# Kernel optimization log

Hardware: AMD Instinct MI355X
Metric: run time of the kernel (lower is better)

## Reference

```python
import jax, jax.numpy as jnp
import numpy as np

N_NODES = 131072
N_EDGES = 4194304
NUM_GRAPHS = 128


def setup_inputs() -> dict:
    key = jax.random.key(0)
    ks = jax.random.split(key, 12)
    x = jax.random.normal(ks[0], (N_NODES, 3), dtype=jnp.float32)
    edge_index = jax.random.randint(ks[1], (2, N_EDGES), 0, N_NODES, dtype=jnp.int32)
    batch = jnp.sort(jax.random.randint(ks[2], (N_NODES,), 0, NUM_GRAPHS, dtype=jnp.int32))
    W1 = jax.random.normal(ks[3], (3, 16), dtype=jnp.float32) * 0.5
    b1 = jax.random.normal(ks[4], (16,), dtype=jnp.float32) * 0.1
    W2 = jax.random.normal(ks[5], (16, 64), dtype=jnp.float32) * 0.25
    b2 = jax.random.normal(ks[6], (64,), dtype=jnp.float32) * 0.1
    fcw1 = jax.random.normal(ks[7], (64, 32), dtype=jnp.float32) * 0.125
    fcb1 = jax.random.normal(ks[8], (32,), dtype=jnp.float32) * 0.1
    fcw2 = jax.random.normal(ks[9], (32, 2), dtype=jnp.float32) * 0.2
    fcb2 = jax.random.normal(ks[10], (2,), dtype=jnp.float32) * 0.1
    return dict(x=x, edge_index=edge_index, batch=batch, W1=W1, b1=b1,
                W2=W2, b2=b2, fcw1=fcw1, fcb1=fcb1, fcw2=fcw2, fcb2=fcb2)


def _gcn_conv(x, W, b, src, dst, n_nodes):
    # PyG GCNConv: add self-loops, symmetric D^-1/2 A_hat D^-1/2, then scatter-add at dst.
    h = x @ W  # [N, out]
    deg = jax.ops.segment_sum(jnp.ones_like(dst, dtype=h.dtype), dst, num_segments=n_nodes)
    dinv = jnp.where(deg > 0, jax.lax.rsqrt(jnp.maximum(deg, 1.0)), 0.0)
    norm = dinv[src] * dinv[dst]  # [E]
    msgs = norm[:, None] * h[src]  # gather + scale, [E, out]
    return jax.ops.segment_sum(msgs, dst, num_segments=n_nodes) + b


def reference(x, edge_index, batch, W1, b1, W2, b2, fcw1, fcb1, fcw2, fcb2):
    n = x.shape[0]
    loop = jnp.arange(n, dtype=edge_index.dtype)
    src = jnp.concatenate([edge_index[0], loop])
    dst = jnp.concatenate([edge_index[1], loop])
    h = jax.nn.relu(_gcn_conv(x, W1, b1, src, dst, n))
    h = jax.nn.relu(_gcn_conv(h, W2, b2, src, dst, n))
    # global_mean_pool over batch ids
    s = jax.ops.segment_sum(h, batch, num_segments=NUM_GRAPHS)
    cnt = jax.ops.segment_sum(jnp.ones((n,), h.dtype), batch, num_segments=NUM_GRAPHS)
    g = s / jnp.maximum(cnt, 1.0)[:, None]  # [G, 64]
    g = g @ fcw1 + fcb1
    return g @ fcw2 + fcb2  # [G, 2]
```

## Files before the change

### kernel.cpp

```cpp
#include <hip/hip_runtime.h>
#include <hip/hip_fp16.h>

#define N_NODES 131072
#define N_EDGES 4194304
#define NUM_GRAPHS 128

#define NB 1024
#define NPB 128
#define BSHIFT 7
#define BCAP 5120
#define GSPAN 8

typedef int iv4 __attribute__((ext_vector_type(4)));

__device__ __forceinline__ int scan128(int tid, int v, int* wsum) {
  __syncthreads();
  int incl = v;
  #pragma unroll
  for (int d = 1; d < 64; d <<= 1) {
    int t = __shfl_up(incl, d);
    if ((tid & 63) >= d) incl += t;
  }
  if (tid < NPB && (tid & 63) == 63) wsum[tid >> 6] = incl;
  __syncthreads();
  int base = (tid >= 64 && tid < NPB) ? wsum[0] : 0;
  return base + incl - v;
}

__global__ __launch_bounds__(1024) void k_binfill(const iv4* __restrict__ src4,
                                                  const iv4* __restrict__ dst4,
                                                  int* __restrict__ bcount,
                                                  unsigned* __restrict__ binned) {
  __shared__ int base_[NB], rank_[NB];
  for (int k = threadIdx.x; k < NB; k += 1024) rank_[k] = 0;
  __syncthreads();
  unsigned pk[16];
  int bk[16], rr[16];
  int q0 = blockIdx.x * 4096 + threadIdx.x;
  #pragma unroll
  for (int i = 0; i < 4; ++i) {
    iv4 sv = __builtin_nontemporal_load(&src4[q0 + i * 1024]);
    iv4 dv = __builtin_nontemporal_load(&dst4[q0 + i * 1024]);
    #pragma unroll
    for (int j = 0; j < 4; ++j) {
      int idx = i * 4 + j;
      int s = sv[j], d = dv[j];
      bk[idx] = d >> BSHIFT;
      pk[idx] = ((unsigned)s << BSHIFT) | (unsigned)(d & (NPB - 1));
      rr[idx] = atomicAdd(&rank_[bk[idx]], 1);
    }
  }
  __syncthreads();
  for (int k = threadIdx.x; k < NB; k += 1024)
    base_[k] = k * BCAP + atomicAdd(&bcount[k], rank_[k]);
  __syncthreads();
  #pragma unroll
  for (int i = 0; i < 16; ++i)
    binned[base_[bk[i]] + rr[i]] = pk[i];
}

__global__ __launch_bounds__(512) void k_prep(const unsigned* __restrict__ binned,
                                              const int* __restrict__ bcount,
                                              const float* __restrict__ x,
                                              float* __restrict__ dinv,
                                              float4* __restrict__ xs4) {
  __shared__ int dcount[NPB];
  int tid = threadIdx.x;
  if (tid < NPB) dcount[tid] = 0;
  __syncthreads();
  int b = blockIdx.x;
  int s0 = b * BCAP;
  int n = bcount[b];
  for (int e = tid; e < n; e += 512) {
    unsigned ent = __builtin_nontemporal_load(&binned[s0 + e]);
    atomicAdd(&dcount[ent & (NPB - 1)], 1);
  }
  __syncthreads();
  if (tid < NPB) {
    int node = b * NPB + tid;
    float di = rsqrtf((float)(dcount[tid] + 1));
    dinv[node] = di;
    xs4[node] = make_float4(di * x[node * 3 + 0], di * x[node * 3 + 1],
                            di * x[node * 3 + 2], 0.f);
  }
}

__global__ __launch_bounds__(512) void k_sagg3h1(const unsigned* __restrict__ binned,
                                                 const int* __restrict__ bcount,
                                                 const float* __restrict__ xs,
                                                 const float4* __restrict__ xs4,
                                                 const float* __restrict__ dinv,
                                                 const float* __restrict__ W1,
                                                 const float* __restrict__ b1,
                                                 unsigned* __restrict__ h1h) {
  __shared__ int dcount[NPB], cursor[NPB], nbase[NPB];
  __shared__ int wsum[2];
  __shared__ int csrL[BCAP];
  __shared__ float w[48];
  __shared__ float bb[16];
  __shared__ float accS[NPB * 4];
  int tid = threadIdx.x;
  if (tid >= 256 && tid < 304) w[tid - 256] = W1[tid - 256];
  if (tid >= 320 && tid < 336) bb[tid - 320] = b1[tid - 320];
  if (tid < NPB) dcount[tid] = 0;
  __syncthreads();

  int b = blockIdx.x;
  int s0 = b * BCAP;
  int n = bcount[b];
  unsigned ent_r[10];
  #pragma unroll
  for (int j = 0; j < 10; ++j) {
    int e = tid + j * 512;
    if (e < n) {
      unsigned ent = __builtin_nontemporal_load(&binned[s0 + e]);
      ent_r[j] = ent;
      atomicAdd(&dcount[ent & (NPB - 1)], 1);
    }
  }
  __syncthreads();

  int v = (tid < NPB) ? dcount[tid] : 0;
  int pref = scan128(tid, v, wsum);
  if (tid < NPB) { cursor[tid] = pref; nbase[tid] = pref; }
  __syncthreads();

  #pragma unroll
  for (int j = 0; j < 10; ++j) {
    int e = tid + j * 512;
    if (e < n) {
      unsigned ent = ent_r[j];
      int pos = atomicAdd(&cursor[ent & (NPB - 1)], 1);
      csrL[pos] = (int)(ent >> BSHIFT) << 4;
    }
  }
  __syncthreads();

  int dl = tid >> 2;
  int q = tid & 3;
  int node = b * NPB + dl;
  int off = nbase[dl];
  int len = dcount[dl];
  const char* xsc = (const char*)xs;
  int qb = q << 2;
  float acc = 0.f;
  #pragma unroll 4
  for (int k = 0; k < len; ++k) {
    int bo = csrL[off + k];
    acc += *(const float*)(xsc + bo + qb);
  }
  accS[tid] = acc;
  __syncthreads();

  float di = dinv[node];
  float4 xself = xs4[node];
  float a0 = di * (accS[dl * 4 + 0] + xself.x);
  float a1 = di * (accS[dl * 4 + 1] + xself.y);
  float a2 = di * (accS[dl * 4 + 2] + xself.z);
  float o[4];
  #pragma unroll
  for (int j = 0; j < 4; ++j) {
    int cc = q * 4 + j;
    float vv = a0 * w[cc] + a1 * w[16 + cc] + a2 * w[32 + cc] + bb[cc];
    o[j] = di * fmaxf(vv, 0.f);
  }
  __half2 p0 = __floats2half2_rn(o[0], o[1]);
  __half2 p1 = __floats2half2_rn(o[2], o[3]);
  uint2 st;
  st.x = *reinterpret_cast<unsigned*>(&p0);
  st.y = *reinterpret_cast<unsigned*>(&p1);
  *(uint2*)(h1h + (size_t)node * 8 + q * 2) = st;
}

__global__ __launch_bounds__(512) void k_sagg16pool(const unsigned* __restrict__ binned,
                                                    const int* __restrict__ bcount,
                                                    const unsigned* __restrict__ h1h,
                                                    const float* __restrict__ dinv,
                                                    const int* __restrict__ batch,
                                                    const float* __restrict__ W2,
                                                    const float* __restrict__ b2,
                                                    float* __restrict__ gsum) {
  __shared__ int dcount[NPB], cursor[NPB], nbase[NPB];
  __shared__ int wsum[2];
  __shared__ int csrL[BCAP];
  __shared__ float aggS[NPB * 16];
  __shared__ float w2s[1024];
  __shared__ float b2s[64];
  __shared__ float gacc[GSPAN * 64];
  int tid = threadIdx.x;
  w2s[tid] = W2[tid];
  w2s[tid + 512] = W2[tid + 512];
  if (tid < 64) b2s[tid] = b2[tid];
  if (tid < GSPAN * 64) gacc[tid] = 0.f;
  if (tid < NPB) dcount[tid] = 0;
  __syncthreads();

  int b = blockIdx.x;
  int s0 = b * BCAP;
  int n = bcount[b];
  unsigned ent_r[10];
  #pragma unroll
  for (int j = 0; j < 10; ++j) {
    int e = tid + j * 512;
    if (e < n) {
      unsigned ent = __builtin_nontemporal_load(&binned[s0 + e]);
      ent_r[j] = ent;
      atomicAdd(&dcount[ent & (NPB - 1)], 1);
    }
  }
  __syncthreads();

  int v = (tid < NPB) ? dcount[tid] : 0;
  int pref = scan128(tid, v, wsum);
  if (tid < NPB) { cursor[tid] = pref; nbase[tid] = pref; }
  __syncthreads();

  #pragma unroll
  for (int j = 0; j < 10; ++j) {
    int e = tid + j * 512;
    if (e < n) {
      unsigned ent = ent_r[j];
      int pos = atomicAdd(&cursor[ent & (NPB - 1)], 1);
      csrL[pos] = (int)(ent >> BSHIFT) << 5;
    }
  }
  __syncthreads();

  const char* h1c = (const char*)h1h;
  int dl = tid >> 2;
  int q = tid & 3;
  int qb = q << 3;
  int node = b * NPB + dl;
  int off = nbase[dl];
  int len = dcount[dl];
  float o0 = 0.f, o1 = 0.f, o2 = 0.f, o3 = 0.f;
  #pragma unroll 4
  for (int k = 0; k < len; ++k) {
    int bo = csrL[off + k];
    uint2 hv = *(const uint2*)(h1c + bo + qb);
    __half2 p0 = *reinterpret_cast<const __half2*>(&hv.x);
    __half2 p1 = *reinterpret_cast<const __half2*>(&hv.y);
    o0 += __low2float(p0); o1 += __high2float(p0);
    o2 += __low2float(p1); o3 += __high2float(p1);
  }
  float di = dinv[node];
  uint2 sv = *(const uint2*)(h1h + (size_t)node * 8 + q * 2);
  __half2 s0h = *reinterpret_cast<const __half2*>(&sv.x);
  __half2 s1h = *reinterpret_cast<const __half2*>(&sv.y);
  aggS[dl * 16 + q * 4 + 0] = di * (o0 + __low2float(s0h));
  aggS[dl * 16 + q * 4 + 1] = di * (o1 + __high2float(s0h));
  aggS[dl * 16 + q * 4 + 2] = di * (o2 + __low2float(s1h));
  aggS[dl * 16 + q * 4 + 3] = di * (o3 + __high2float(s1h));
  __syncthreads();

  int c = tid & 63;
  int slot = tid >> 6;
  int g0 = batch[b * NPB];
  float racc = 0.f;
  int curli = -1;
  for (int nloc = slot; nloc < NPB; nloc += 8) {
    int nd = b * NPB + nloc;
    int li = batch[nd] - g0;
    if (li != curli) {
      if (curli >= 0) {
        if (curli < GSPAN) atomicAdd(&gacc[curli * 64 + c], racc);
        else atomicAdd(&gsum[(size_t)(g0 + curli) * 64 + c], racc);
      }
      curli = li;
      racc = 0.f;
    }
    float vv = b2s[c];
    const float* ar = &aggS[nloc * 16];
    #pragma unroll
    for (int k = 0; k < 16; ++k) vv += ar[k] * w2s[k * 64 + c];
    racc += fmaxf(vv, 0.f);
  }
  if (curli >= 0) {
    if (curli < GSPAN) atomicAdd(&gacc[curli * 64 + c], racc);
    else atomicAdd(&gsum[(size_t)(g0 + curli) * 64 + c], racc);
  }
  __syncthreads();

  int span = batch[b * NPB + NPB - 1] - g0 + 1;
  if (span > GSPAN) span = GSPAN;
  for (int li = tid >> 6; li < span; li += 8) {
    atomicAdd(&gsum[(size_t)(g0 + li) * 64 + c], gacc[li * 64 + c]);
  }
}

__global__ __launch_bounds__(64) void k_fc(const float* __restrict__ gsum,
                                           const int* __restrict__ batch,
                                           const float* __restrict__ fcw1,
                                           const float* __restrict__ fcb1,
                                           const float* __restrict__ fcw2,
                                           const float* __restrict__ fcb2,
                                           float* __restrict__ out) {
  int g = blockIdx.x;
  int lo = 0, hi = N_NODES;
  while (lo < hi) { int m = (lo + hi) >> 1; if (batch[m] < g) lo = m + 1; else hi = m; }
  int start = lo;
  lo = start; hi = N_NODES;
  while (lo < hi) { int m = (lo + hi) >> 1; if (batch[m] < g + 1) lo = m + 1; else hi = m; }
  float inv = 1.0f / fmaxf((float)(lo - start), 1.0f);

  __shared__ float gmean[64];
  gmean[threadIdx.x] = gsum[(size_t)g * 64 + threadIdx.x] * inv;
  __syncthreads();

  __shared__ float hid[32];
  if (threadIdx.x < 32) {
    float a = fcb1[threadIdx.x];
    #pragma unroll
    for (int k = 0; k < 64; ++k) a += gmean[k] * fcw1[k * 32 + threadIdx.x];
    hid[threadIdx.x] = a;
  }
  __syncthreads();

  if (threadIdx.x < 2) {
    float a = fcb2[threadIdx.x];
    #pragma unroll
    for (int k = 0; k < 32; ++k) a += hid[k] * fcw2[k * 2 + threadIdx.x];
    out[g * 2 + threadIdx.x] = a;
  }
}

extern "C" void kernel_launch(void* const* d_in, const int* in_sizes, int n_in,
                              void* d_out, int out_size, void* d_ws, size_t ws_size,
                              hipStream_t stream) {
  const float* x    = (const float*)d_in[0];
  const int*   ei   = (const int*)d_in[1];
  const int*   batch= (const int*)d_in[2];
  const float* W1   = (const float*)d_in[3];
  const float* b1   = (const float*)d_in[4];
  const float* W2   = (const float*)d_in[5];
  const float* b2   = (const float*)d_in[6];
  const float* fcw1 = (const float*)d_in[7];
  const float* fcb1 = (const float*)d_in[8];
  const float* fcw2 = (const float*)d_in[9];
  const float* fcb2 = (const float*)d_in[10];
  float* out = (float*)d_out;

  char* w = (char*)d_ws;
  size_t off = 0;
  auto alloc = [&](size_t bytes) {
    void* p = w + off;
    off += (bytes + 255) & ~(size_t)255;
    return p;
  };
  float*    gsum    = (float*)   alloc((size_t)NUM_GRAPHS * 64 * 4);
  int*      bcount  = (int*)     alloc((size_t)NB * 4);
  unsigned* binned  = (unsigned*)alloc((size_t)NB * BCAP * 4);
  float*    dinv    = (float*)   alloc((size_t)N_NODES * 4);
  float4*   xs4     = (float4*)  alloc((size_t)N_NODES * 16);
  unsigned* h1h     = (unsigned*)alloc((size_t)N_NODES * 32);

  const iv4* src4 = (const iv4*)ei;
  const iv4* dst4 = (const iv4*)(ei + N_EDGES);

  (void)hipMemsetAsync(gsum, 0, (size_t)NUM_GRAPHS * 64 * 4 + (size_t)NB * 4, stream);
  k_binfill<<<N_EDGES / 16384, 1024, 0, stream>>>(src4, dst4, bcount, binned);
  k_prep<<<NB, 512, 0, stream>>>(binned, bcount, x, dinv, xs4);
  k_sagg3h1<<<NB, 512, 0, stream>>>(binned, bcount, (const float*)xs4, xs4, dinv, W1, b1, h1h);
  k_sagg16pool<<<NB, 512, 0, stream>>>(binned, bcount, h1h, dinv, batch, W2, b2, gsum);
  k_fc<<<NUM_GRAPHS, 64, 0, stream>>>(gsum, batch, fcw1, fcb1, fcw2, fcb2, out);
}
```

Measured before the change: 135.0 us.

## Use 256-node bins with half-bin blocks and recompute dinv from local degree

Doubles the bin size to 256 destination nodes (512 bins) so binfill writes fewer, larger bins. The aggregation kernels now launch two blocks per bin, and each block filters the entries belonging to its 128-node half. The dinv array is dropped and recomputed from the per-node degree, and the layer-2 gather uses 8 lanes per node with 4-byte loads. In exchange, each aggregation block reads the whole bin and discards about half of it, which doubles edge-list read traffic in those kernels.

```diff
diff --git a/kernel.cpp b/kernel.cpp
--- a/kernel.cpp
+++ b/kernel.cpp
@@ -5,10 +5,12 @@
 #define N_EDGES 4194304
 #define NUM_GRAPHS 128
 
-#define NB 1024
-#define NPB 128
-#define BSHIFT 7
-#define BCAP 5120
+#define NB 512
+#define NPB 256
+#define BSHIFT 8
+#define BCAP 10240
+#define HNPB 128
+#define HCAP 5632
 #define GSPAN 8
 
 typedef int iv4 __attribute__((ext_vector_type(4)));
@@ -21,9 +23,9 @@
     int t = __shfl_up(incl, d);
     if ((tid & 63) >= d) incl += t;
   }
-  if (tid < NPB && (tid & 63) == 63) wsum[tid >> 6] = incl;
-  __syncthreads();
-  int base = (tid >= 64 && tid < NPB) ? wsum[0] : 0;
+  if (tid < HNPB && (tid & 63) == 63) wsum[tid >> 6] = incl;
+  __syncthreads();
+  int base = (tid >= 64 && tid < HNPB) ? wsum[0] : 0;
   return base + incl - v;
 }
 
@@ -59,11 +61,10 @@
     binned[base_[bk[i]] + rr[i]] = pk[i];
 }
 
-__global__ __launch_bounds__(512) void k_prep(const unsigned* __restrict__ binned,
-                                              const int* __restrict__ bcount,
-                                              const float* __restrict__ x,
-                                              float* __restrict__ dinv,
-                                              float4* __restrict__ xs4) {
+__global__ __launch_bounds__(1024) void k_prep(const unsigned* __restrict__ binned,
+                                               const int* __restrict__ bcount,
+                                               const float* __restrict__ x,
+                                               float4* __restrict__ xs4) {
   __shared__ int dcount[NPB];
   int tid = threadIdx.x;
   if (tid < NPB) dcount[tid] = 0;
@@ -71,7 +72,7 @@
   int b = blockIdx.x;
   int s0 = b * BCAP;
   int n = bcount[b];
-  for (int e = tid; e < n; e += 512) {
+  for (int e = tid; e < n; e += 1024) {
     unsigned ent = __builtin_nontemporal_load(&binned[s0 + e]);
     atomicAdd(&dcount[ent & (NPB - 1)], 1);
   }
@@ -79,7 +80,6 @@
   if (tid < NPB) {
     int node = b * NPB + tid;
     float di = rsqrtf((float)(dcount[tid] + 1));
-    dinv[node] = di;
     xs4[node] = make_float4(di * x[node * 3 + 0], di * x[node * 3 + 1],
                             di * x[node * 3 + 2], 0.f);
   }
@@ -89,48 +89,50 @@
                                                  const int* __restrict__ bcount,
                                                  const float* __restrict__ xs,
                                                  const float4* __restrict__ xs4,
-                                                 const float* __restrict__ dinv,
                                                  const float* __restrict__ W1,
                                                  const float* __restrict__ b1,
                                                  unsigned* __restrict__ h1h) {
-  __shared__ int dcount[NPB], cursor[NPB], nbase[NPB];
+  __shared__ int dcount[HNPB], cursor[HNPB], nbase[HNPB];
   __shared__ int wsum[2];
-  __shared__ int csrL[BCAP];
+  __shared__ int csrL[HCAP];
   __shared__ float w[48];
   __shared__ float bb[16];
-  __shared__ float accS[NPB * 4];
+  __shared__ float accS[HNPB * 4];
   int tid = threadIdx.x;
   if (tid >= 256 && tid < 304) w[tid - 256] = W1[tid - 256];
   if (tid >= 320 && tid < 336) bb[tid - 320] = b1[tid - 320];
-  if (tid < NPB) dcount[tid] = 0;
-  __syncthreads();
-
-  int b = blockIdx.x;
+  if (tid < HNPB) dcount[tid] = 0;
+  __syncthreads();
+
+  int b = blockIdx.x >> 1;
+  int half = blockIdx.x & 1;
+  int hbit = half << 7;
   int s0 = b * BCAP;
   int n = bcount[b];
-  unsigned ent_r[10];
-  #pragma unroll
-  for (int j = 0; j < 10; ++j) {
+  unsigned ent_r[20];
+  #pragma unroll
+  for (int j = 0; j < 20; ++j) {
     int e = tid + j * 512;
+    unsigned ent = 0xFFFFFFFFu;
     if (e < n) {
-      unsigned ent = __builtin_nontemporal_load(&binned[s0 + e]);
-      ent_r[j] = ent;
-      atomicAdd(&dcount[ent & (NPB - 1)], 1);
-    }
-  }
-  __syncthreads();
-
-  int v = (tid < NPB) ? dcount[tid] : 0;
+      ent = __builtin_nontemporal_load(&binned[s0 + e]);
+      if (((int)ent & 128) == hbit) atomicAdd(&dcount[ent & (HNPB - 1)], 1);
+      else ent = 0xFFFFFFFFu;
+    }
+    ent_r[j] = ent;
+  }
+  __syncthreads();
+
+  int v = (tid < HNPB) ? dcount[tid] : 0;
   int pref = scan128(tid, v, wsum);
-  if (tid < NPB) { cursor[tid] = pref; nbase[tid] = pref; }
-  __syncthreads();
-
-  #pragma unroll
-  for (int j = 0; j < 10; ++j) {
-    int e = tid + j * 512;
-    if (e < n) {
-      unsigned ent = ent_r[j];
-      int pos = atomicAdd(&cursor[ent & (NPB - 1)], 1);
+  if (tid < HNPB) { cursor[tid] = pref; nbase[tid] = pref; }
+  __syncthreads();
+
+  #pragma unroll
+  for (int j = 0; j < 20; ++j) {
+    unsigned ent = ent_r[j];
+    if (ent != 0xFFFFFFFFu) {
+      int pos = atomicAdd(&cursor[ent & (HNPB - 1)], 1);
       csrL[pos] = (int)(ent >> BSHIFT) << 4;
     }
   }
@@ -138,7 +140,7 @@
 
   int dl = tid >> 2;
   int q = tid & 3;
-  int node = b * NPB + dl;
+  int node = b * NPB + hbit + dl;
   int off = nbase[dl];
   int len = dcount[dl];
   const char* xsc = (const char*)xs;
@@ -152,7 +154,7 @@
   accS[tid] = acc;
   __syncthreads();
 
-  float di = dinv[node];
+  float di = rsqrtf((float)(len + 1));
   float4 xself = xs4[node];
   float a0 = di * (accS[dl * 4 + 0] + xself.x);
   float a1 = di * (accS[dl * 4 + 1] + xself.y);
@@ -172,95 +174,92 @@
   *(uint2*)(h1h + (size_t)node * 8 + q * 2) = st;
 }
 
-__global__ __launch_bounds__(512) void k_sagg16pool(const unsigned* __restrict__ binned,
-                                                    const int* __restrict__ bcount,
-                                                    const unsigned* __restrict__ h1h,
-                                                    const float* __restrict__ dinv,
-                                                    const int* __restrict__ batch,
-                                                    const float* __restrict__ W2,
-                                                    const float* __restrict__ b2,
-                                                    float* __restrict__ gsum) {
-  __shared__ int dcount[NPB], cursor[NPB], nbase[NPB];
+__global__ __launch_bounds__(1024) void k_sagg16pool(const unsigned* __restrict__ binned,
+                                                     const int* __restrict__ bcount,
+                                                     const unsigned* __restrict__ h1h,
+                                                     const int* __restrict__ batch,
+                                                     const float* __restrict__ W2,
+                                                     const float* __restrict__ b2,
+                                                     float* __restrict__ gsum) {
+  __shared__ int dcount[HNPB], cursor[HNPB], nbase[HNPB];
   __shared__ int wsum[2];
-  __shared__ int csrL[BCAP];
-  __shared__ float aggS[NPB * 16];
+  __shared__ int csrL[HCAP];
+  __shared__ float aggS[HNPB * 16];
   __shared__ float w2s[1024];
   __shared__ float b2s[64];
   __shared__ float gacc[GSPAN * 64];
   int tid = threadIdx.x;
   w2s[tid] = W2[tid];
-  w2s[tid + 512] = W2[tid + 512];
   if (tid < 64) b2s[tid] = b2[tid];
   if (tid < GSPAN * 64) gacc[tid] = 0.f;
-  if (tid < NPB) dcount[tid] = 0;
-  __syncthreads();
-
-  int b = blockIdx.x;
+  if (tid < HNPB) dcount[tid] = 0;
+  __syncthreads();
+
+  int b = blockIdx.x >> 1;
+  int half = blockIdx.x & 1;
+  int hbit = half << 7;
   int s0 = b * BCAP;
   int n = bcount[b];
   unsigned ent_r[10];
   #pragma unroll
   for (int j = 0; j < 10; ++j) {
-    int e = tid + j * 512;
+    int e = tid + j * 1024;
+    unsigned ent = 0xFFFFFFFFu;
     if (e < n) {
-      unsigned ent = __builtin_nontemporal_load(&binned[s0 + e]);
-      ent_r[j] = ent;
-      atomicAdd(&dcount[ent & (NPB - 1)], 1);
-    }
-  }
-  __syncthreads();
-
-  int v = (tid < NPB) ? dcount[tid] : 0;
+      ent = __builtin_nontemporal_load(&binned[s0 + e]);
+      if (((int)ent & 128) == hbit) atomicAdd(&dcount[ent & (HNPB - 1)], 1);
+      else ent = 0xFFFFFFFFu;
+    }
+    ent_r[j] = ent;
+  }
+  __syncthreads();
+
+  int v = (tid < HNPB) ? dcount[tid] : 0;
   int pref = scan128(tid, v, wsum);
-  if (tid < NPB) { cursor[tid] = pref; nbase[tid] = pref; }
+  if (tid < HNPB) { cursor[tid] = pref; nbase[tid] = pref; }
   __syncthreads();
 
   #pragma unroll
   for (int j = 0; j < 10; ++j) {
-    int e = tid + j * 512;
-    if (e < n) {
-      unsigned ent = ent_r[j];
-      int pos = atomicAdd(&cursor[ent & (NPB - 1)], 1);
+    unsigned ent = ent_r[j];
+    if (ent != 0xFFFFFFFFu) {
+      int pos = atomicAdd(&cursor[ent & (HNPB - 1)], 1);
       csrL[pos] = (int)(ent >> BSHIFT) << 5;
     }
   }
   __syncthreads();
 
   const char* h1c = (const char*)h1h;
-  int dl = tid >> 2;
-  int q = tid & 3;
-  int qb = q << 3;
-  int node = b * NPB + dl;
+  int q = tid & 7;
+  int qb = q << 2;
+  int dl = tid >> 3;
+  int node = b * NPB + hbit + dl;
   int off = nbase[dl];
   int len = dcount[dl];
-  float o0 = 0.f, o1 = 0.f, o2 = 0.f, o3 = 0.f;
-  #pragma unroll 4
+  float o0 = 0.f, o1 = 0.f;
+  #pragma unroll 8
   for (int k = 0; k < len; ++k) {
     int bo = csrL[off + k];
-    uint2 hv = *(const uint2*)(h1c + bo + qb);
-    __half2 p0 = *reinterpret_cast<const __half2*>(&hv.x);
-    __half2 p1 = *reinterpret_cast<const __half2*>(&hv.y);
-    o0 += __low2float(p0); o1 += __high2float(p0);
-    o2 += __low2float(p1); o3 += __high2float(p1);
-  }
-  float di = dinv[node];
-  uint2 sv = *(const uint2*)(h1h + (size_t)node * 8 + q * 2);
-  __half2 s0h = *reinterpret_cast<const __half2*>(&sv.x);
-  __half2 s1h = *reinterpret_cast<const __half2*>(&sv.y);
-  aggS[dl * 16 + q * 4 + 0] = di * (o0 + __low2float(s0h));
-  aggS[dl * 16 + q * 4 + 1] = di * (o1 + __high2float(s0h));
-  aggS[dl * 16 + q * 4 + 2] = di * (o2 + __low2float(s1h));
-  aggS[dl * 16 + q * 4 + 3] = di * (o3 + __high2float(s1h));
+    unsigned hv = *(const unsigned*)(h1c + bo + qb);
+    __half2 p = *reinterpret_cast<const __half2*>(&hv);
+    o0 += __low2float(p);
+    o1 += __high2float(p);
+  }
+  float di = rsqrtf((float)(len + 1));
+  unsigned sv = h1h[(size_t)node * 8 + q];
+  __half2 sh = *reinterpret_cast<const __half2*>(&sv);
+  aggS[dl * 16 + 2 * q + 0] = di * (o0 + __low2float(sh));
+  aggS[dl * 16 + 2 * q + 1] = di * (o1 + __high2float(sh));
   __syncthreads();
 
   int c = tid & 63;
   int slot = tid >> 6;
-  int g0 = batch[b * NPB];
+  int nodebase = b * NPB + hbit;
+  int g0 = batch[nodebase];
   float racc = 0.f;
   int curli = -1;
-  for (int nloc = slot; nloc < NPB; nloc += 8) {
-    int nd = b * NPB + nloc;
-    int li = batch[nd] - g0;
+  for (int nloc = slot; nloc < HNPB; nloc += 16) {
+    int li = batch[nodebase + nloc] - g0;
     if (li != curli) {
       if (curli >= 0) {
         if (curli < GSPAN) atomicAdd(&gacc[curli * 64 + c], racc);
@@ -281,9 +280,9 @@
   }
   __syncthreads();
 
-  int span = batch[b * NPB + NPB - 1] - g0 + 1;
+  int span = batch[nodebase + HNPB - 1] - g0 + 1;
   if (span > GSPAN) span = GSPAN;
-  for (int li = tid >> 6; li < span; li += 8) {
+  for (int li = tid >> 6; li < span; li += 16) {
     atomicAdd(&gsum[(size_t)(g0 + li) * 64 + c], gacc[li * 64 + c]);
   }
 }
@@ -350,7 +349,6 @@
   float*    gsum    = (float*)   alloc((size_t)NUM_GRAPHS * 64 * 4);
   int*      bcount  = (int*)     alloc((size_t)NB * 4);
   unsigned* binned  = (unsigned*)alloc((size_t)NB * BCAP * 4);
-  float*    dinv    = (float*)   alloc((size_t)N_NODES * 4);
   float4*   xs4     = (float4*)  alloc((size_t)N_NODES * 16);
   unsigned* h1h     = (unsigned*)alloc((size_t)N_NODES * 32);
 
@@ -359,8 +357,8 @@
 
   (void)hipMemsetAsync(gsum, 0, (size_t)NUM_GRAPHS * 64 * 4 + (size_t)NB * 4, stream);
   k_binfill<<<N_EDGES / 16384, 1024, 0, stream>>>(src4, dst4, bcount, binned);
-  k_prep<<<NB, 512, 0, stream>>>(binned, bcount, x, dinv, xs4);
-  k_sagg3h1<<<NB, 512, 0, stream>>>(binned, bcount, (const float*)xs4, xs4, dinv, W1, b1, h1h);
-  k_sagg16pool<<<NB, 512, 0, stream>>>(binned, bcount, h1h, dinv, batch, W2, b2, gsum);
+  k_prep<<<NB, 1024, 0, stream>>>(binned, bcount, x, xs4);
+  k_sagg3h1<<<NB * 2, 512, 0, stream>>>(binned, bcount, (const float*)xs4, xs4, W1, b1, h1h);
+  k_sagg16pool<<<NB * 2, 1024, 0, stream>>>(binned, bcount, h1h, batch, W2, b2, gsum);
   k_fc<<<NUM_GRAPHS, 64, 0, stream>>>(gsum, batch, fcw1, fcb1, fcw2, fcb2, out);
 }
```

Result: slower. 139.5 us (+3.3%).

## Fuse prep and both aggregation stages into one cooperative kernel with grid syncs

Applied to the files above, without the earlier changes.

Replaces the three per-bin kernels (prep, layer-1 aggregation, layer-2 aggregation plus pooling) with one cooperative kernel. Each block builds its shared-memory CSR once and keeps it across two grid-wide syncs, instead of re-reading the binned edges and rebuilding the CSR in every kernel. Bins grow to 256 destination nodes (512 blocks), and the dinv buffer is dropped in favour of recomputing rsqrt from the local degree counts. This adds grid-sync cost, more shared memory per block and more register pressure. A fallback launch path with 1024-thread versions of the separate kernels is kept in case the cooperative launch fails.

```diff
diff --git a/kernel.cpp b/kernel.cpp
--- a/kernel.cpp
+++ b/kernel.cpp
@@ -1,31 +1,20 @@
 #include <hip/hip_runtime.h>
 #include <hip/hip_fp16.h>
+#include <hip/hip_cooperative_groups.h>
+
+namespace cg = cooperative_groups;
 
 #define N_NODES 131072
 #define N_EDGES 4194304
 #define NUM_GRAPHS 128
 
-#define NB 1024
-#define NPB 128
-#define BSHIFT 7
-#define BCAP 5120
+#define NB 512
+#define NPB 256
+#define BSHIFT 8
+#define BCAP 10240
 #define GSPAN 8
 
 typedef int iv4 __attribute__((ext_vector_type(4)));
-
-__device__ __forceinline__ int scan128(int tid, int v, int* wsum) {
-  __syncthreads();
-  int incl = v;
-  #pragma unroll
-  for (int d = 1; d < 64; d <<= 1) {
-    int t = __shfl_up(incl, d);
-    if ((tid & 63) >= d) incl += t;
-  }
-  if (tid < NPB && (tid & 63) == 63) wsum[tid >> 6] = incl;
-  __syncthreads();
-  int base = (tid >= 64 && tid < NPB) ? wsum[0] : 0;
-  return base + incl - v;
-}
 
 __global__ __launch_bounds__(1024) void k_binfill(const iv4* __restrict__ src4,
                                                   const iv4* __restrict__ dst4,
@@ -59,11 +48,240 @@
     binned[base_[bk[i]] + rr[i]] = pk[i];
 }
 
-__global__ __launch_bounds__(512) void k_prep(const unsigned* __restrict__ binned,
-                                              const int* __restrict__ bcount,
-                                              const float* __restrict__ x,
-                                              float* __restrict__ dinv,
-                                              float4* __restrict__ xs4) {
+__global__ __launch_bounds__(512, 4) void k_fused(const unsigned* __restrict__ binned,
+                                                  const int* __restrict__ bcount,
+                                                  const float* __restrict__ x,
+                                                  const int* __restrict__ batch,
+                                                  const float* __restrict__ W1,
+                                                  const float* __restrict__ b1,
+                                                  const float* __restrict__ W2,
+                                                  const float* __restrict__ b2,
+                                                  float4* __restrict__ xs4,
+                                                  unsigned* __restrict__ h1h,
+                                                  float* __restrict__ gsum) {
+  __shared__ int csrL[BCAP];
+  __shared__ int dcount[NPB], cursor[NPB], nbase[NPB];
+  __shared__ int wsum[4];
+  __shared__ float w1s[48], b1s[16];
+  __shared__ float w2s[1024], b2s[64];
+  __shared__ float gacc[GSPAN * 64];
+  __shared__ float accS[NPB * 4];
+
+  int tid = threadIdx.x;
+  int b = blockIdx.x;
+
+  w2s[tid] = W2[tid];
+  w2s[tid + 512] = W2[tid + 512];
+  if (tid < 48) w1s[tid] = W1[tid];
+  if (tid >= 64 && tid < 80) b1s[tid - 64] = b1[tid - 64];
+  if (tid >= 128 && tid < 192) b2s[tid - 128] = b2[tid - 128];
+  gacc[tid] = 0.f;
+  if (tid < NPB) dcount[tid] = 0;
+  __syncthreads();
+
+  int s0 = b * BCAP;
+  int n = bcount[b];
+  unsigned ent_r[20];
+  #pragma unroll
+  for (int j = 0; j < 20; ++j) {
+    int e = tid + j * 512;
+    if (e < n) {
+      unsigned ent = __builtin_nontemporal_load(&binned[s0 + e]);
+      ent_r[j] = ent;
+      atomicAdd(&dcount[ent & (NPB - 1)], 1);
+    }
+  }
+  __syncthreads();
+
+  int v = (tid < NPB) ? dcount[tid] : 0;
+  {
+    int incl = v;
+    #pragma unroll
+    for (int d = 1; d < 64; d <<= 1) {
+      int t = __shfl_up(incl, d);
+      if ((tid & 63) >= d) incl += t;
+    }
+    if (tid < NPB && (tid & 63) == 63) wsum[tid >> 6] = incl;
+    __syncthreads();
+    if (tid < NPB) {
+      int base = 0;
+      int wv = tid >> 6;
+      for (int w2 = 0; w2 < wv; ++w2) base += wsum[w2];
+      int pref = base + incl - v;
+      cursor[tid] = pref;
+      nbase[tid] = pref;
+    }
+  }
+  __syncthreads();
+
+  #pragma unroll
+  for (int j = 0; j < 20; ++j) {
+    int e = tid + j * 512;
+    if (e < n) {
+      unsigned ent = ent_r[j];
+      int pos = atomicAdd(&cursor[ent & (NPB - 1)], 1);
+      csrL[pos] = (int)(ent >> BSHIFT) << 4;
+    }
+  }
+
+  if (tid < NPB) {
+    int node = b * NPB + tid;
+    float di = rsqrtf((float)(dcount[tid] + 1));
+    xs4[node] = make_float4(di * x[node * 3 + 0], di * x[node * 3 + 1],
+                            di * x[node * 3 + 2], 0.f);
+  }
+  __threadfence();
+  cg::this_grid().sync();
+
+  {
+    const char* xsc = (const char*)xs4;
+    int q = tid & 3;
+    int qb = q << 2;
+    int dl0 = tid >> 2;
+    #pragma unroll
+    for (int pass = 0; pass < 2; ++pass) {
+      int dl = dl0 + pass * 128;
+      int off = nbase[dl], len = dcount[dl];
+      float acc = 0.f;
+      #pragma unroll 4
+      for (int k = 0; k < len; ++k) {
+        int bo = csrL[off + k];
+        acc += *(const float*)(xsc + bo + qb);
+      }
+      accS[dl * 4 + q] = acc;
+    }
+    __syncthreads();
+    #pragma unroll
+    for (int pass = 0; pass < 2; ++pass) {
+      int dl = dl0 + pass * 128;
+      int node = b * NPB + dl;
+      int len = dcount[dl];
+      float di = rsqrtf((float)(len + 1));
+      float4 xself = xs4[node];
+      float a0 = di * (accS[dl * 4 + 0] + xself.x);
+      float a1 = di * (accS[dl * 4 + 1] + xself.y);
+      float a2 = di * (accS[dl * 4 + 2] + xself.z);
+      float o[4];
+      #pragma unroll
+      for (int j = 0; j < 4; ++j) {
+        int cc = q * 4 + j;
+        float vv = a0 * w1s[cc] + a1 * w1s[16 + cc] + a2 * w1s[32 + cc] + b1s[cc];
+        o[j] = di * fmaxf(vv, 0.f);
+      }
+      __half2 p0 = __floats2half2_rn(o[0], o[1]);
+      __half2 p1 = __floats2half2_rn(o[2], o[3]);
+      uint2 st;
+      st.x = *reinterpret_cast<unsigned*>(&p0);
+      st.y = *reinterpret_cast<unsigned*>(&p1);
+      *(uint2*)(h1h + (size_t)node * 8 + q * 2) = st;
+    }
+  }
+  __threadfence();
+  cg::this_grid().sync();
+
+  {
+    const char* h1c = (const char*)h1h;
+    int q = tid & 3;
+    int qb = q << 3;
+    int dl0 = tid >> 2;
+    float pa0, pa1, pa2, pa3, qa0, qa1, qa2, qa3;
+    {
+      int node = b * NPB + dl0;
+      int off = nbase[dl0], len = dcount[dl0];
+      float o0 = 0.f, o1 = 0.f, o2 = 0.f, o3 = 0.f;
+      #pragma unroll 4
+      for (int k = 0; k < len; ++k) {
+        int bo = csrL[off + k] << 1;
+        uint2 hv = *(const uint2*)(h1c + bo + qb);
+        __half2 p0 = *reinterpret_cast<const __half2*>(&hv.x);
+        __half2 p1 = *reinterpret_cast<const __half2*>(&hv.y);
+        o0 += __low2float(p0); o1 += __high2float(p0);
+        o2 += __low2float(p1); o3 += __high2float(p1);
+      }
+      float di = rsqrtf((float)(len + 1));
+      uint2 sv = *(const uint2*)(h1h + (size_t)node * 8 + q * 2);
+      __half2 s0h = *reinterpret_cast<const __half2*>(&sv.x);
+      __half2 s1h = *reinterpret_cast<const __half2*>(&sv.y);
+      pa0 = di * (o0 + __low2float(s0h));
+      pa1 = di * (o1 + __high2float(s0h));
+      pa2 = di * (o2 + __low2float(s1h));
+      pa3 = di * (o3 + __high2float(s1h));
+    }
+    {
+      int dl = dl0 + 128;
+      int node = b * NPB + dl;
+      int off = nbase[dl], len = dcount[dl];
+      float o0 = 0.f, o1 = 0.f, o2 = 0.f, o3 = 0.f;
+      #pragma unroll 4
+      for (int k = 0; k < len; ++k) {
+        int bo = csrL[off + k] << 1;
+        uint2 hv = *(const uint2*)(h1c + bo + qb);
+        __half2 p0 = *reinterpret_cast<const __half2*>(&hv.x);
+        __half2 p1 = *reinterpret_cast<const __half2*>(&hv.y);
+        o0 += __low2float(p0); o1 += __high2float(p0);
+        o2 += __low2float(p1); o3 += __high2float(p1);
+      }
+      float di = rsqrtf((float)(len + 1));
+      uint2 sv = *(const uint2*)(h1h + (size_t)node * 8 + q * 2);
+      __half2 s0h = *reinterpret_cast<const __half2*>(&sv.x);
+      __half2 s1h = *reinterpret_cast<const __half2*>(&sv.y);
+      qa0 = di * (o0 + __low2float(s0h));
+      qa1 = di * (o1 + __high2float(s0h));
+      qa2 = di * (o2 + __low2float(s1h));
+      qa3 = di * (o3 + __high2float(s1h));
+    }
+    __syncthreads();
+    float* aggS = (float*)csrL;
+    aggS[dl0 * 16 + q * 4 + 0] = pa0;
+    aggS[dl0 * 16 + q * 4 + 1] = pa1;
+    aggS[dl0 * 16 + q * 4 + 2] = pa2;
+    aggS[dl0 * 16 + q * 4 + 3] = pa3;
+    int dl1 = dl0 + 128;
+    aggS[dl1 * 16 + q * 4 + 0] = qa0;
+    aggS[dl1 * 16 + q * 4 + 1] = qa1;
+    aggS[dl1 * 16 + q * 4 + 2] = qa2;
+    aggS[dl1 * 16 + q * 4 + 3] = qa3;
+    __syncthreads();
+
+    int c = tid & 63;
+    int slot = tid >> 6;
+    int g0 = batch[b * NPB];
+    float racc = 0.f;
+    int curli = -1;
+    for (int nloc = slot; nloc < NPB; nloc += 8) {
+      int li = batch[b * NPB + nloc] - g0;
+      if (li != curli) {
+        if (curli >= 0) {
+          if (curli < GSPAN) atomicAdd(&gacc[curli * 64 + c], racc);
+          else atomicAdd(&gsum[(size_t)(g0 + curli) * 64 + c], racc);
+        }
+        curli = li;
+        racc = 0.f;
+      }
+      float vv = b2s[c];
+      const float* ar = &aggS[nloc * 16];
+      #pragma unroll
+      for (int k = 0; k < 16; ++k) vv += ar[k] * w2s[k * 64 + c];
+      racc += fmaxf(vv, 0.f);
+    }
+    if (curli >= 0) {
+      if (curli < GSPAN) atomicAdd(&gacc[curli * 64 + c], racc);
+      else atomicAdd(&gsum[(size_t)(g0 + curli) * 64 + c], racc);
+    }
+    __syncthreads();
+
+    int span = batch[b * NPB + NPB - 1] - g0 + 1;
+    if (span > GSPAN) span = GSPAN;
+    for (int li = tid >> 6; li < span; li += 8)
+      atomicAdd(&gsum[(size_t)(g0 + li) * 64 + c], gacc[li * 64 + c]);
+  }
+}
+
+
+__global__ __launch_bounds__(1024) void k_prep(const unsigned* __restrict__ binned,
+                                               const int* __restrict__ bcount,
+                                               const float* __restrict__ x,
+                                               float4* __restrict__ xs4) {
   __shared__ int dcount[NPB];
   int tid = threadIdx.x;
   if (tid < NPB) dcount[tid] = 0;
@@ -71,7 +289,7 @@
   int b = blockIdx.x;
   int s0 = b * BCAP;
   int n = bcount[b];
-  for (int e = tid; e < n; e += 512) {
+  for (int e = tid; e < n; e += 1024) {
     unsigned ent = __builtin_nontemporal_load(&binned[s0 + e]);
     atomicAdd(&dcount[ent & (NPB - 1)], 1);
   }
@@ -79,29 +297,27 @@
   if (tid < NPB) {
     int node = b * NPB + tid;
     float di = rsqrtf((float)(dcount[tid] + 1));
-    dinv[node] = di;
     xs4[node] = make_float4(di * x[node * 3 + 0], di * x[node * 3 + 1],
                             di * x[node * 3 + 2], 0.f);
   }
 }
 
-__global__ __launch_bounds__(512) void k_sagg3h1(const unsigned* __restrict__ binned,
-                                                 const int* __restrict__ bcount,
-                                                 const float* __restrict__ xs,
-                                                 const float4* __restrict__ xs4,
-                                                 const float* __restrict__ dinv,
-                                                 const float* __restrict__ W1,
-                                                 const float* __restrict__ b1,
-                                                 unsigned* __restrict__ h1h) {
+__global__ __launch_bounds__(1024) void k_fb3h1(const unsigned* __restrict__ binned,
+                                                const int* __restrict__ bcount,
+                                                const float* __restrict__ xs,
+                                                const float4* __restrict__ xs4,
+                                                const float* __restrict__ W1,
+                                                const float* __restrict__ b1,
+                                                unsigned* __restrict__ h1h) {
   __shared__ int dcount[NPB], cursor[NPB], nbase[NPB];
-  __shared__ int wsum[2];
+  __shared__ int wsum[4];
   __shared__ int csrL[BCAP];
   __shared__ float w[48];
   __shared__ float bb[16];
   __shared__ float accS[NPB * 4];
   int tid = threadIdx.x;
-  if (tid >= 256 && tid < 304) w[tid - 256] = W1[tid - 256];
-  if (tid >= 320 && tid < 336) bb[tid - 320] = b1[tid - 320];
+  if (tid >= 512 && tid < 560) w[tid - 512] = W1[tid - 512];
+  if (tid >= 576 && tid < 592) bb[tid - 576] = b1[tid - 576];
   if (tid < NPB) dcount[tid] = 0;
   __syncthreads();
 
@@ -111,7 +327,7 @@
   unsigned ent_r[10];
   #pragma unroll
   for (int j = 0; j < 10; ++j) {
-    int e = tid + j * 512;
+    int e = tid + j * 1024;
     if (e < n) {
       unsigned ent = __builtin_nontemporal_load(&binned[s0 + e]);
       ent_r[j] = ent;
@@ -121,13 +337,29 @@
   __syncthreads();
 
   int v = (tid < NPB) ? dcount[tid] : 0;
-  int pref = scan128(tid, v, wsum);
-  if (tid < NPB) { cursor[tid] = pref; nbase[tid] = pref; }
+  {
+    int incl = v;
+    #pragma unroll
+    for (int d = 1; d < 64; d <<= 1) {
+      int t = __shfl_up(incl, d);
+      if ((tid & 63) >= d) incl += t;
+    }
+    if (tid < NPB && (tid & 63) == 63) wsum[tid >> 6] = incl;
+    __syncthreads();
+    if (tid < NPB) {
+      int base = 0;
+      int wv = tid >> 6;
+      for (int w2 = 0; w2 < wv; ++w2) base += wsum[w2];
+      int pref = base + incl - v;
+      cursor[tid] = pref;
+      nbase[tid] = pref;
+    }
+  }
   __syncthreads();
 
   #pragma unroll
   for (int j = 0; j < 10; ++j) {
-    int e = tid + j * 512;
+    int e = tid + j * 1024;
     if (e < n) {
       unsigned ent = ent_r[j];
       int pos = atomicAdd(&cursor[ent & (NPB - 1)], 1);
@@ -152,7 +384,7 @@
   accS[tid] = acc;
   __syncthreads();
 
-  float di = dinv[node];
+  float di = rsqrtf((float)(len + 1));
   float4 xself = xs4[node];
   float a0 = di * (accS[dl * 4 + 0] + xself.x);
   float a1 = di * (accS[dl * 4 + 1] + xself.y);
@@ -172,24 +404,21 @@
   *(uint2*)(h1h + (size_t)node * 8 + q * 2) = st;
 }
 
-__global__ __launch_bounds__(512) void k_sagg16pool(const unsigned* __restrict__ binned,
-                                                    const int* __restrict__ bcount,
-                                                    const unsigned* __restrict__ h1h,
-                                                    const float* __restrict__ dinv,
-                                                    const int* __restrict__ batch,
-                                                    const float* __restrict__ W2,
-                                                    const float* __restrict__ b2,
-                                                    float* __restrict__ gsum) {
+__global__ __launch_bounds__(1024) void k_fb16pool(const unsigned* __restrict__ binned,
+                                                   const int* __restrict__ bcount,
+                                                   const unsigned* __restrict__ h1h,
+                                                   const int* __restrict__ batch,
+                                                   const float* __restrict__ W2,
+                                                   const float* __restrict__ b2,
+                                                   float* __restrict__ gsum) {
   __shared__ int dcount[NPB], cursor[NPB], nbase[NPB];
-  __shared__ int wsum[2];
+  __shared__ int wsum[4];
   __shared__ int csrL[BCAP];
-  __shared__ float aggS[NPB * 16];
   __shared__ float w2s[1024];
   __shared__ float b2s[64];
   __shared__ float gacc[GSPAN * 64];
   int tid = threadIdx.x;
   w2s[tid] = W2[tid];
-  w2s[tid + 512] = W2[tid + 512];
   if (tid < 64) b2s[tid] = b2[tid];
   if (tid < GSPAN * 64) gacc[tid] = 0.f;
   if (tid < NPB) dcount[tid] = 0;
@@ -201,7 +430,7 @@
   unsigned ent_r[10];
   #pragma unroll
   for (int j = 0; j < 10; ++j) {
-    int e = tid + j * 512;
+    int e = tid + j * 1024;
     if (e < n) {
       unsigned ent = __builtin_nontemporal_load(&binned[s0 + e]);
       ent_r[j] = ent;
@@ -211,13 +440,29 @@
   __syncthreads();
 
   int v = (tid < NPB) ? dcount[tid] : 0;
-  int pref = scan128(tid, v, wsum);
-  if (tid < NPB) { cursor[tid] = pref; nbase[tid] = pref; }
+  {
+    int incl = v;
+    #pragma unroll
+    for (int d = 1; d < 64; d <<= 1) {
+      int t = __shfl_up(incl, d);
+      if ((tid & 63) >= d) incl += t;
+    }
+    if (tid < NPB && (tid & 63) == 63) wsum[tid >> 6] = incl;
+    __syncthreads();
+    if (tid < NPB) {
+      int base = 0;
+      int wv = tid >> 6;
+      for (int w2 = 0; w2 < wv; ++w2) base += wsum[w2];
+      int pref = base + incl - v;
+      cursor[tid] = pref;
+      nbase[tid] = pref;
+    }
+  }
   __syncthreads();
 
   #pragma unroll
   for (int j = 0; j < 10; ++j) {
-    int e = tid + j * 512;
+    int e = tid + j * 1024;
     if (e < n) {
       unsigned ent = ent_r[j];
       int pos = atomicAdd(&cursor[ent & (NPB - 1)], 1);
@@ -243,14 +488,20 @@
     o0 += __low2float(p0); o1 += __high2float(p0);
     o2 += __low2float(p1); o3 += __high2float(p1);
   }
-  float di = dinv[node];
+  float di = rsqrtf((float)(len + 1));
   uint2 sv = *(const uint2*)(h1h + (size_t)node * 8 + q * 2);
   __half2 s0h = *reinterpret_cast<const __half2*>(&sv.x);
   __half2 s1h = *reinterpret_cast<const __half2*>(&sv.y);
-  aggS[dl * 16 + q * 4 + 0] = di * (o0 + __low2float(s0h));
-  aggS[dl * 16 + q * 4 + 1] = di * (o1 + __high2float(s0h));
-  aggS[dl * 16 + q * 4 + 2] = di * (o2 + __low2float(s1h));
-  aggS[dl * 16 + q * 4 + 3] = di * (o3 + __high2float(s1h));
+  o0 = di * (o0 + __low2float(s0h));
+  o1 = di * (o1 + __high2float(s0h));
+  o2 = di * (o2 + __low2float(s1h));
+  o3 = di * (o3 + __high2float(s1h));
+  __syncthreads();
+  float* aggS = (float*)csrL;
+  aggS[dl * 16 + q * 4 + 0] = o0;
+  aggS[dl * 16 + q * 4 + 1] = o1;
+  aggS[dl * 16 + q * 4 + 2] = o2;
+  aggS[dl * 16 + q * 4 + 3] = o3;
   __syncthreads();
 
   int c = tid & 63;
@@ -258,9 +509,8 @@
   int g0 = batch[b * NPB];
   float racc = 0.f;
   int curli = -1;
-  for (int nloc = slot; nloc < NPB; nloc += 8) {
-    int nd = b * NPB + nloc;
-    int li = batch[nd] - g0;
+  for (int nloc = slot; nloc < NPB; nloc += 16) {
+    int li = batch[b * NPB + nloc] - g0;
     if (li != curli) {
       if (curli >= 0) {
         if (curli < GSPAN) atomicAdd(&gacc[curli * 64 + c], racc);
@@ -283,9 +533,8 @@
 
   int span = batch[b * NPB + NPB - 1] - g0 + 1;
   if (span > GSPAN) span = GSPAN;
-  for (int li = tid >> 6; li < span; li += 8) {
+  for (int li = tid >> 6; li < span; li += 16)
     atomicAdd(&gsum[(size_t)(g0 + li) * 64 + c], gacc[li * 64 + c]);
-  }
 }
 
 __global__ __launch_bounds__(64) void k_fc(const float* __restrict__ gsum,
@@ -350,7 +599,6 @@
   float*    gsum    = (float*)   alloc((size_t)NUM_GRAPHS * 64 * 4);
   int*      bcount  = (int*)     alloc((size_t)NB * 4);
   unsigned* binned  = (unsigned*)alloc((size_t)NB * BCAP * 4);
-  float*    dinv    = (float*)   alloc((size_t)N_NODES * 4);
   float4*   xs4     = (float4*)  alloc((size_t)N_NODES * 16);
   unsigned* h1h     = (unsigned*)alloc((size_t)N_NODES * 32);
 
@@ -359,8 +607,17 @@
 
   (void)hipMemsetAsync(gsum, 0, (size_t)NUM_GRAPHS * 64 * 4 + (size_t)NB * 4, stream);
   k_binfill<<<N_EDGES / 16384, 1024, 0, stream>>>(src4, dst4, bcount, binned);
-  k_prep<<<NB, 512, 0, stream>>>(binned, bcount, x, dinv, xs4);
-  k_sagg3h1<<<NB, 512, 0, stream>>>(binned, bcount, (const float*)xs4, xs4, dinv, W1, b1, h1h);
-  k_sagg16pool<<<NB, 512, 0, stream>>>(binned, bcount, h1h, dinv, batch, W2, b2, gsum);
+
+  void* args[] = {(void*)&binned, (void*)&bcount, (void*)&x, (void*)&batch,
+                  (void*)&W1, (void*)&b1, (void*)&W2, (void*)&b2,
+                  (void*)&xs4, (void*)&h1h, (void*)&gsum};
+  hipError_t ce = hipLaunchCooperativeKernel((const void*)k_fused, dim3(NB),
+                                             dim3(512), args, 0, stream);
+  if (ce != hipSuccess) {
+    k_prep<<<NB, 1024, 0, stream>>>(binned, bcount, x, xs4);
+    k_fb3h1<<<NB, 1024, 0, stream>>>(binned, bcount, (const float*)xs4, xs4, W1, b1, h1h);
+    k_fb16pool<<<NB, 1024, 0, stream>>>(binned, bcount, h1h, batch, W2, b2, gsum);
+  }
+
   k_fc<<<NUM_GRAPHS, 64, 0, stream>>>(gsum, batch, fcw1, fcb1, fcw2, fcb2, out);
 }
```

After: 374.7 us. +177.7%, slower.

## Double bin size to 256 nodes per block, recompute dinv, register-cache W2

Applied to the files above, without the earlier changes.

Bins now hold 256 destination nodes with 1024-thread blocks instead of 128 nodes and 512 threads, which halves the block count and changes the prefix scan to span four wavefronts. The dinv array is removed, and each kernel recomputes the normalisation from the local degree count. In the pooling stage each thread keeps its W2 column in registers and reads aggregated rows as float4. The larger bins raise LDS and register use per block, and the fixed 10-entry per-thread edge buffer (10240 capacity) still has to cover the worst-case bin size.

```diff
diff --git a/kernel.cpp b/kernel.cpp
--- a/kernel.cpp
+++ b/kernel.cpp
@@ -5,27 +5,13 @@
 #define N_EDGES 4194304
 #define NUM_GRAPHS 128
 
-#define NB 1024
-#define NPB 128
-#define BSHIFT 7
-#define BCAP 5120
+#define NB 512
+#define NPB 256
+#define BSHIFT 8
+#define BCAP 10240
 #define GSPAN 8
 
 typedef int iv4 __attribute__((ext_vector_type(4)));
-
-__device__ __forceinline__ int scan128(int tid, int v, int* wsum) {
-  __syncthreads();
-  int incl = v;
-  #pragma unroll
-  for (int d = 1; d < 64; d <<= 1) {
-    int t = __shfl_up(incl, d);
-    if ((tid & 63) >= d) incl += t;
-  }
-  if (tid < NPB && (tid & 63) == 63) wsum[tid >> 6] = incl;
-  __syncthreads();
-  int base = (tid >= 64 && tid < NPB) ? wsum[0] : 0;
-  return base + incl - v;
-}
 
 __global__ __launch_bounds__(1024) void k_binfill(const iv4* __restrict__ src4,
                                                   const iv4* __restrict__ dst4,
@@ -59,11 +45,10 @@
     binned[base_[bk[i]] + rr[i]] = pk[i];
 }
 
-__global__ __launch_bounds__(512) void k_prep(const unsigned* __restrict__ binned,
-                                              const int* __restrict__ bcount,
-                                              const float* __restrict__ x,
-                                              float* __restrict__ dinv,
-                                              float4* __restrict__ xs4) {
+__global__ __launch_bounds__(1024) void k_prep(const unsigned* __restrict__ binned,
+                                               const int* __restrict__ bcount,
+                                               const float* __restrict__ x,
+                                               float4* __restrict__ xs4) {
   __shared__ int dcount[NPB];
   int tid = threadIdx.x;
   if (tid < NPB) dcount[tid] = 0;
@@ -71,7 +56,7 @@
   int b = blockIdx.x;
   int s0 = b * BCAP;
   int n = bcount[b];
-  for (int e = tid; e < n; e += 512) {
+  for (int e = tid; e < n; e += 1024) {
     unsigned ent = __builtin_nontemporal_load(&binned[s0 + e]);
     atomicAdd(&dcount[ent & (NPB - 1)], 1);
   }
@@ -79,29 +64,27 @@
   if (tid < NPB) {
     int node = b * NPB + tid;
     float di = rsqrtf((float)(dcount[tid] + 1));
-    dinv[node] = di;
     xs4[node] = make_float4(di * x[node * 3 + 0], di * x[node * 3 + 1],
                             di * x[node * 3 + 2], 0.f);
   }
 }
 
-__global__ __launch_bounds__(512) void k_sagg3h1(const unsigned* __restrict__ binned,
-                                                 const int* __restrict__ bcount,
-                                                 const float* __restrict__ xs,
-                                                 const float4* __restrict__ xs4,
-                                                 const float* __restrict__ dinv,
-                                                 const float* __restrict__ W1,
-                                                 const float* __restrict__ b1,
-                                                 unsigned* __restrict__ h1h) {
+__global__ __launch_bounds__(1024) void k_sagg3h1(const unsigned* __restrict__ binned,
+                                                  const int* __restrict__ bcount,
+                                                  const float* __restrict__ xs,
+                                                  const float4* __restrict__ xs4,
+                                                  const float* __restrict__ W1,
+                                                  const float* __restrict__ b1,
+                                                  unsigned* __restrict__ h1h) {
   __shared__ int dcount[NPB], cursor[NPB], nbase[NPB];
-  __shared__ int wsum[2];
+  __shared__ int wsum[4];
   __shared__ int csrL[BCAP];
   __shared__ float w[48];
   __shared__ float bb[16];
   __shared__ float accS[NPB * 4];
   int tid = threadIdx.x;
-  if (tid >= 256 && tid < 304) w[tid - 256] = W1[tid - 256];
-  if (tid >= 320 && tid < 336) bb[tid - 320] = b1[tid - 320];
+  if (tid >= 512 && tid < 560) w[tid - 512] = W1[tid - 512];
+  if (tid >= 576 && tid < 592) bb[tid - 576] = b1[tid - 576];
   if (tid < NPB) dcount[tid] = 0;
   __syncthreads();
 
@@ -111,7 +94,7 @@
   unsigned ent_r[10];
   #pragma unroll
   for (int j = 0; j < 10; ++j) {
-    int e = tid + j * 512;
+    int e = tid + j * 1024;
     if (e < n) {
       unsigned ent = __builtin_nontemporal_load(&binned[s0 + e]);
       ent_r[j] = ent;
@@ -121,13 +104,29 @@
   __syncthreads();
 
   int v = (tid < NPB) ? dcount[tid] : 0;
-  int pref = scan128(tid, v, wsum);
-  if (tid < NPB) { cursor[tid] = pref; nbase[tid] = pref; }
+  {
+    int incl = v;
+    #pragma unroll
+    for (int d = 1; d < 64; d <<= 1) {
+      int t = __shfl_up(incl, d);
+      if ((tid & 63) >= d) incl += t;
+    }
+    if (tid < NPB && (tid & 63) == 63) wsum[tid >> 6] = incl;
+    __syncthreads();
+    if (tid < NPB) {
+      int base = 0;
+      int wv = tid >> 6;
+      for (int w2 = 0; w2 < wv; ++w2) base += wsum[w2];
+      int pref = base + incl - v;
+      cursor[tid] = pref;
+      nbase[tid] = pref;
+    }
+  }
   __syncthreads();
 
   #pragma unroll
   for (int j = 0; j < 10; ++j) {
-    int e = tid + j * 512;
+    int e = tid + j * 1024;
     if (e < n) {
       unsigned ent = ent_r[j];
       int pos = atomicAdd(&cursor[ent & (NPB - 1)], 1);
@@ -152,7 +151,7 @@
   accS[tid] = acc;
   __syncthreads();
 
-  float di = dinv[node];
+  float di = rsqrtf((float)(len + 1));
   float4 xself = xs4[node];
   float a0 = di * (accS[dl * 4 + 0] + xself.x);
   float a1 = di * (accS[dl * 4 + 1] + xself.y);
@@ -172,24 +171,22 @@
   *(uint2*)(h1h + (size_t)node * 8 + q * 2) = st;
 }
 
-__global__ __launch_bounds__(512) void k_sagg16pool(const unsigned* __restrict__ binned,
-                                                    const int* __restrict__ bcount,
-                                                    const unsigned* __restrict__ h1h,
-                                                    const float* __restrict__ dinv,
-                                                    const int* __restrict__ batch,
-                                                    const float* __restrict__ W2,
-                                                    const float* __restrict__ b2,
-                                                    float* __restrict__ gsum) {
+__global__ __launch_bounds__(1024) void k_sagg16pool(const unsigned* __restrict__ binned,
+                                                     const int* __restrict__ bcount,
+                                                     const unsigned* __restrict__ h1h,
+                                                     const int* __restrict__ batch,
+                                                     const float* __restrict__ W2,
+                                                     const float* __restrict__ b2,
+                                                     float* __restrict__ gsum) {
   __shared__ int dcount[NPB], cursor[NPB], nbase[NPB];
-  __shared__ int wsum[2];
+  __shared__ int wsum[4];
   __shared__ int csrL[BCAP];
-  __shared__ float aggS[NPB * 16];
+  __shared__ __attribute__((aligned(16))) float aggS[NPB * 16];
   __shared__ float w2s[1024];
   __shared__ float b2s[64];
   __shared__ float gacc[GSPAN * 64];
   int tid = threadIdx.x;
   w2s[tid] = W2[tid];
-  w2s[tid + 512] = W2[tid + 512];
   if (tid < 64) b2s[tid] = b2[tid];
   if (tid < GSPAN * 64) gacc[tid] = 0.f;
   if (tid < NPB) dcount[tid] = 0;
@@ -201,7 +198,7 @@
   unsigned ent_r[10];
   #pragma unroll
   for (int j = 0; j < 10; ++j) {
-    int e = tid + j * 512;
+    int e = tid + j * 1024;
     if (e < n) {
       unsigned ent = __builtin_nontemporal_load(&binned[s0 + e]);
       ent_r[j] = ent;
@@ -211,13 +208,29 @@
   __syncthreads();
 
   int v = (tid < NPB) ? dcount[tid] : 0;
-  int pref = scan128(tid, v, wsum);
-  if (tid < NPB) { cursor[tid] = pref; nbase[tid] = pref; }
+  {
+    int incl = v;
+    #pragma unroll
+    for (int d = 1; d < 64; d <<= 1) {
+      int t = __shfl_up(incl, d);
+      if ((tid & 63) >= d) incl += t;
+    }
+    if (tid < NPB && (tid & 63) == 63) wsum[tid >> 6] = incl;
+    __syncthreads();
+    if (tid < NPB) {
+      int base = 0;
+      int wv = tid >> 6;
+      for (int w2 = 0; w2 < wv; ++w2) base += wsum[w2];
+      int pref = base + incl - v;
+      cursor[tid] = pref;
+      nbase[tid] = pref;
+    }
+  }
   __syncthreads();
 
   #pragma unroll
   for (int j = 0; j < 10; ++j) {
-    int e = tid + j * 512;
+    int e = tid + j * 1024;
     if (e < n) {
       unsigned ent = ent_r[j];
       int pos = atomicAdd(&cursor[ent & (NPB - 1)], 1);
@@ -243,7 +256,7 @@
     o0 += __low2float(p0); o1 += __high2float(p0);
     o2 += __low2float(p1); o3 += __high2float(p1);
   }
-  float di = dinv[node];
+  float di = rsqrtf((float)(len + 1));
   uint2 sv = *(const uint2*)(h1h + (size_t)node * 8 + q * 2);
   __half2 s0h = *reinterpret_cast<const __half2*>(&sv.x);
   __half2 s1h = *reinterpret_cast<const __half2*>(&sv.y);
@@ -254,13 +267,18 @@
   __syncthreads();
 
   int c = tid & 63;
+  float w2r[16];
+  #pragma unroll
+  for (int k = 0; k < 16; ++k) w2r[k] = w2s[k * 64 + c];
+  float bc = b2s[c];
+
   int slot = tid >> 6;
   int g0 = batch[b * NPB];
   float racc = 0.f;
   int curli = -1;
-  for (int nloc = slot; nloc < NPB; nloc += 8) {
-    int nd = b * NPB + nloc;
-    int li = batch[nd] - g0;
+  const float4* aggS4 = (const float4*)aggS;
+  for (int nloc = slot; nloc < NPB; nloc += 16) {
+    int li = batch[b * NPB + nloc] - g0;
     if (li != curli) {
       if (curli >= 0) {
         if (curli < GSPAN) atomicAdd(&gacc[curli * 64 + c], racc);
@@ -269,10 +287,15 @@
       curli = li;
       racc = 0.f;
     }
-    float vv = b2s[c];
-    const float* ar = &aggS[nloc * 16];
-    #pragma unroll
-    for (int k = 0; k < 16; ++k) vv += ar[k] * w2s[k * 64 + c];
+    float4 a0 = aggS4[nloc * 4 + 0];
+    float4 a1 = aggS4[nloc * 4 + 1];
+    float4 a2 = aggS4[nloc * 4 + 2];
+    float4 a3 = aggS4[nloc * 4 + 3];
+    float vv = bc;
+    vv += a0.x * w2r[0]  + a0.y * w2r[1]  + a0.z * w2r[2]  + a0.w * w2r[3];
+    vv += a1.x * w2r[4]  + a1.y * w2r[5]  + a1.z * w2r[6]  + a1.w * w2r[7];
+    vv += a2.x * w2r[8]  + a2.y * w2r[9]  + a2.z * w2r[10] + a2.w * w2r[11];
+    vv += a3.x * w2r[12] + a3.y * w2r[13] + a3.z * w2r[14] + a3.w * w2r[15];
     racc += fmaxf(vv, 0.f);
   }
   if (curli >= 0) {
@@ -283,7 +306,7 @@
 
   int span = batch[b * NPB + NPB - 1] - g0 + 1;
   if (span > GSPAN) span = GSPAN;
-  for (int li = tid >> 6; li < span; li += 8) {
+  for (int li = tid >> 6; li < span; li += 16) {
     atomicAdd(&gsum[(size_t)(g0 + li) * 64 + c], gacc[li * 64 + c]);
   }
 }
@@ -350,7 +373,6 @@
   float*    gsum    = (float*)   alloc((size_t)NUM_GRAPHS * 64 * 4);
   int*      bcount  = (int*)     alloc((size_t)NB * 4);
   unsigned* binned  = (unsigned*)alloc((size_t)NB * BCAP * 4);
-  float*    dinv    = (float*)   alloc((size_t)N_NODES * 4);
   float4*   xs4     = (float4*)  alloc((size_t)N_NODES * 16);
   unsigned* h1h     = (unsigned*)alloc((size_t)N_NODES * 32);
 
@@ -359,8 +381,8 @@
 
   (void)hipMemsetAsync(gsum, 0, (size_t)NUM_GRAPHS * 64 * 4 + (size_t)NB * 4, stream);
   k_binfill<<<N_EDGES / 16384, 1024, 0, stream>>>(src4, dst4, bcount, binned);
-  k_prep<<<NB, 512, 0, stream>>>(binned, bcount, x, dinv, xs4);
-  k_sagg3h1<<<NB, 512, 0, stream>>>(binned, bcount, (const float*)xs4, xs4, dinv, W1, b1, h1h);
-  k_sagg16pool<<<NB, 512, 0, stream>>>(binned, bcount, h1h, dinv, batch, W2, b2, gsum);
+  k_prep<<<NB, 1024, 0, stream>>>(binned, bcount, x, xs4);
+  k_sagg3h1<<<NB, 1024, 0, stream>>>(binned, bcount, (const float*)xs4, xs4, W1, b1, h1h);
+  k_sagg16pool<<<NB, 1024, 0, stream>>>(binned, bcount, h1h, batch, W2, b2, gsum);
   k_fc<<<NUM_GRAPHS, 64, 0, stream>>>(gsum, batch, fcw1, fcb1, fcw2, fcb2, out);
 }
```

Result: faster. 121.6 us (-9.9%).
